# Kernel optimization log

Hardware: AMD Instinct MI355X
Metric: run time of the kernel (lower is better)

## Reference

```python
import jax, jax.numpy as jnp
import numpy as np

B, C, H, W = 2, 512, 64, 64
TC = 256  # transform_channels


def _w(k, o, i):
    return jax.random.normal(k, (o, i), jnp.float32) * (1.0 / np.sqrt(i))


def setup_inputs() -> dict:
    key = jax.random.key(0)
    ks = jax.random.split(key, 8)
    ones = lambda n: jnp.ones((n,), jnp.float32)
    zeros = lambda n: jnp.zeros((n,), jnp.float32)
    return {
        "x": jax.random.normal(ks[0], (B, C, H, W), jnp.float32),
        "q_w1": _w(ks[1], TC, C), "q_g1": ones(TC), "q_b1": zeros(TC),
        "q_w2": _w(ks[2], TC, TC), "q_g2": ones(TC), "q_b2": zeros(TC),
        "k_w1": _w(ks[3], TC, 2 * C), "k_g1": ones(TC), "k_b1": zeros(TC),
        "k_w2": _w(ks[4], TC, TC), "k_g2": ones(TC), "k_b2": zeros(TC),
        "v_w": _w(ks[5], TC, 2 * C), "v_g": ones(TC), "v_b": zeros(TC),
        "o_w": _w(ks[6], C, TC), "o_g": ones(C), "o_b": zeros(C),
    }


def _proj(x, w, g, b):
    """1x1 conv (bias-free) + eval-mode BN (mean=0,var=1 -> per-ch affine) + ReLU.
    x: (B, Cin, N) -> (B, Cout, N)"""
    y = jnp.einsum('oc,bcn->bon', w, x)
    return jax.nn.relu(y * g[None, :, None] + b[None, :, None])


def reference(x, q_w1, q_g1, q_b1, q_w2, q_g2, q_b2,
              k_w1, k_g1, k_b1, k_w2, k_g2, k_b2,
              v_w, v_g, v_b, o_w, o_g, o_b):
    b, c, h, w = x.shape
    n = h * w
    xf = x.reshape(b, c, n)
    # image-level context: spatial softmax * feats, averaged over all positions
    g_vec = jnp.mean(jax.nn.softmax(xf, axis=2) * xf, axis=2)        # (b, c)
    g_map = jnp.broadcast_to(g_vec[:, :, None], (b, c, n))           # 1x1 bilinear upsample == broadcast
    kv_in = jnp.concatenate([g_map, xf], axis=1)                     # (b, 2c, n)

    q = _proj(_proj(xf, q_w1, q_g1, q_b1), q_w2, q_g2, q_b2)         # (b, tc, n)
    k = _proj(_proj(kv_in, k_w1, k_g1, k_b1), k_w2, k_g2, k_b2)      # (b, tc, n)
    v = _proj(kv_in, v_w, v_g, v_b)                                  # (b, tc, n)

    tc = q.shape[1]
    sim = jnp.einsum('bcn,bcm->bnm', q, k) * (tc ** -0.5)            # (b, n, n)
    attn = jax.nn.softmax(sim, axis=-1)
    ctx = jnp.einsum('bnm,bcm->bcn', attn, v)                        # (b, tc, n)
    out = _proj(ctx, o_w, o_g, o_b)                                  # (b, c, n)
    return out.reshape(b, -1, h, w)
```

## Files before the change

### kernel.cpp

```cpp
#include <hip/hip_runtime.h>
#include <stdint.h>

#define DEVINL __device__ __forceinline__

typedef short s16x8 __attribute__((ext_vector_type(8)));
typedef short s16x4 __attribute__((ext_vector_type(4)));
typedef float f32x4 __attribute__((ext_vector_type(4)));
typedef int   i32x4 __attribute__((ext_vector_type(4)));

DEVINL f32x4 MFMA16(s16x8 a, s16x8 b, f32x4 c) {
  return __builtin_amdgcn_mfma_f32_16x16x32_bf16(a, b, c, 0, 0, 0);
}

DEVINL short f2bf(float f) {
  uint32_t u = __float_as_uint(f);
  uint32_t r = (u + 0x7fffu + ((u >> 16) & 1u)) >> 16;
  return (short)r;
}

DEVINL int packbf(float a, float b) {
  return (int)((uint32_t)(uint16_t)f2bf(a) | ((uint32_t)(uint16_t)f2bf(b) << 16));
}

DEVINL void async16(const void* g, void* l) {
  __builtin_amdgcn_global_load_lds(
      (const __attribute__((address_space(1))) void*)g,
      (__attribute__((address_space(3))) void*)l, 16, 0, 0);
}

DEVINL int ab_off(int row, int kg) {
  return ((row * 128 + kg * 16) ^ ((row & 7) << 4)) >> 1;
}
DEVINL int k_off(int key, int dg) {
  return ((key * 512 + dg * 16) ^ ((key & 7) << 4)) >> 1;
}

__global__ __launch_bounds__(256) void prep_kernel(
    const float* __restrict__ x,
    const float* __restrict__ qw1, const float* __restrict__ qw2,
    const float* __restrict__ kw1, const float* __restrict__ kw2,
    const float* __restrict__ vw, const float* __restrict__ ow,
    short* __restrict__ wbuf, short* __restrict__ xt, float* __restrict__ g) {
  __shared__ float t[32][33];
  int gblk = blockIdx.x, tid = threadIdx.x;
  if (gblk < 2560) {
    int idx = gblk * 256 + tid;
    const float* src; int base, stride, coloff, sh, mask;
    if (idx < 131072)      { src = qw1; base = 0;      stride = 512;  coloff = 0;   sh = 9; mask = 511; }
    else if (idx < 196608) { src = qw2; base = 131072; stride = 256;  coloff = 0;   sh = 8; mask = 255; }
    else if (idx < 327680) { src = kw1; base = 196608; stride = 1024; coloff = 512; sh = 9; mask = 511; }
    else if (idx < 393216) { src = kw2; base = 327680; stride = 256;  coloff = 0;   sh = 8; mask = 255; }
    else if (idx < 524288) { src = vw;  base = 393216; stride = 1024; coloff = 512; sh = 9; mask = 511; }
    else                   { src = ow;  base = 524288; stride = 256;  coloff = 0;   sh = 8; mask = 255; }
    int l = idx - base;
    int r = l >> sh, c = l & mask;
    wbuf[idx] = f2bf(src[(size_t)r * stride + coloff + c]);
  } else if (gblk < 6656) {
    int g2 = gblk - 2560;
    int nt = g2 & 127, ct = (g2 >> 7) & 15, b = g2 >> 11;
    int tx = tid & 31, ty = tid >> 5;
    for (int i = 0; i < 4; ++i) {
      int c = ct * 32 + ty + i * 8;
      t[ty + i * 8][tx] = x[((size_t)(b * 512 + c)) * 4096 + nt * 32 + tx];
    }
    __syncthreads();
    for (int i = 0; i < 4; ++i) {
      int n = nt * 32 + ty + i * 8;
      xt[((size_t)(b * 4096 + n)) * 512 + ct * 32 + tx] = f2bf(t[tx][ty + i * 8]);
    }
  } else {
    int g3 = gblk - 6656;
    int c = g3 & 511, b = g3 >> 9;
    const float* row = x + ((size_t)(b * 512 + c)) * 4096;
    int w = tid >> 6, lane = tid & 63;
    float vals[16];
    float vmax = -3e38f;
    for (int i = 0; i < 4; ++i) {
      float4 v = ((const float4*)row)[tid + i * 256];
      vals[i * 4 + 0] = v.x; vals[i * 4 + 1] = v.y;
      vals[i * 4 + 2] = v.z; vals[i * 4 + 3] = v.w;
    }
    for (int i = 0; i < 16; ++i) vmax = fmaxf(vmax, vals[i]);
    for (int off = 1; off < 64; off <<= 1) vmax = fmaxf(vmax, __shfl_xor(vmax, off));
    float* sb = &t[0][0];
    if (lane == 0) sb[w] = vmax;
    __syncthreads();
    vmax = fmaxf(fmaxf(sb[0], sb[1]), fmaxf(sb[2], sb[3]));
    float se = 0.f, sex = 0.f;
    for (int i = 0; i < 16; ++i) {
      float e = __expf(vals[i] - vmax);
      se += e; sex += e * vals[i];
    }
    for (int off = 1; off < 64; off <<= 1) {
      se += __shfl_xor(se, off);
      sex += __shfl_xor(sex, off);
    }
    __syncthreads();
    if (lane == 0) { sb[4 + w] = se; sb[8 + w] = sex; }
    __syncthreads();
    if (tid == 0) {
      float tse = sb[4] + sb[5] + sb[6] + sb[7];
      float tsx = sb[8] + sb[9] + sb[10] + sb[11];
      g[b * 512 + c] = tsx / (tse * 4096.0f);
    }
  }
}

__global__ __launch_bounds__(64) void bias_kernel(const float* __restrict__ kw1,
                                                  const float* __restrict__ vw,
                                                  const float* __restrict__ g,
                                                  float* __restrict__ kbias,
                                                  float* __restrict__ vbias) {
  int o = blockIdx.x, b = blockIdx.y, which = blockIdx.z;
  const float* W = which ? vw : kw1;
  int lane = threadIdx.x;
  float s = 0.f;
  for (int j = 0; j < 8; ++j) {
    int c = lane + j * 64;
    s += W[(size_t)o * 1024 + c] * g[b * 512 + c];
  }
  for (int off = 1; off < 64; off <<= 1) s += __shfl_xor(s, off);
  if (lane == 0) (which ? vbias : kbias)[b * 256 + o] = s;
}

DEVINL void gemm_core(const short* __restrict__ Ap, const short* __restrict__ Bp,
                      int K, short* Alds, short* Blds, int tid,
                      f32x4 (&acc)[4][2]) {
  int lane = tid & 63, w = tid >> 6, lg = lane >> 4, ln = lane & 15;
  int wm = w & 1, wn = w >> 1;
  int nk = K >> 6;
  for (int kt = 0; kt < nk; ++kt) {
    int k0 = kt * 64;
#pragma unroll
    for (int j = 0; j < 4; ++j) {
      int c = tid + j * 256;
      int row = c >> 3, e = c & 7;
      async16(Ap + (size_t)row * K + k0 + ((e ^ (row & 7)) * 8),
              Alds + (size_t)(c & ~63) * 8);
    }
#pragma unroll
    for (int j = 0; j < 2; ++j) {
      int c = tid + j * 256;
      int row = c >> 3, e = c & 7;
      async16(Bp + (size_t)row * K + k0 + ((e ^ (row & 7)) * 8),
              Blds + (size_t)(c & ~63) * 8);
    }
    __syncthreads();
#pragma unroll
    for (int ks = 0; ks < 2; ++ks) {
      s16x8 af[4], bfr[2];
#pragma unroll
      for (int mi = 0; mi < 4; ++mi)
        af[mi] = *(const s16x8*)(Alds + ab_off(wm * 64 + mi * 16 + ln, ks * 4 + lg));
#pragma unroll
      for (int nj = 0; nj < 2; ++nj)
        bfr[nj] = *(const s16x8*)(Blds + ab_off(wn * 32 + nj * 16 + ln, ks * 4 + lg));
#pragma unroll
      for (int mi = 0; mi < 4; ++mi)
#pragma unroll
        for (int nj = 0; nj < 2; ++nj)
          acc[mi][nj] = MFMA16(af[mi], bfr[nj], acc[mi][nj]);
    }
    __syncthreads();
  }
}

__global__ __launch_bounds__(256) void gemm_l1(
    const short* __restrict__ xt,
    const short* __restrict__ WQ1, const short* __restrict__ WK1,
    const short* __restrict__ WV,
    const float* __restrict__ qg1, const float* __restrict__ qb1,
    const float* __restrict__ kg1, const float* __restrict__ kb1,
    const float* __restrict__ vg, const float* __restrict__ vb,
    const float* __restrict__ kbias, const float* __restrict__ vbias,
    short* __restrict__ t1, short* __restrict__ ctxS, short* __restrict__ vbuf) {
  __shared__ alignas(16) short Alds[8192];
  __shared__ alignas(16) short Blds[4096];
  int nt = blockIdx.x, mt = blockIdx.y;
  int gid = blockIdx.z >> 1, b = blockIdx.z & 1;
  const short* A; const float *gm, *bd, *cb; short* out; bool nmode;
  if (gid == 0)      { A = WQ1; gm = qg1; bd = qb1; cb = nullptr; out = t1;   nmode = true; }
  else if (gid == 1) { A = WK1; gm = kg1; bd = kb1; cb = kbias;   out = ctxS; nmode = true; }
  else               { A = WV;  gm = vg;  bd = vb;  cb = vbias;   out = vbuf; nmode = false; }
  int tid = threadIdx.x, lane = tid & 63, w = tid >> 6, lg = lane >> 4, ln = lane & 15;
  int wm = w & 1, wn = w >> 1;
  f32x4 z = {0.f, 0.f, 0.f, 0.f};
  f32x4 acc[4][2];
  for (int mi = 0; mi < 4; ++mi) for (int nj = 0; nj < 2; ++nj) acc[mi][nj] = z;
  gemm_core(A + (size_t)(mt * 128) * 512, xt + ((size_t)b * 4096 + nt * 64) * 512,
            512, Alds, Blds, tid, acc);
  for (int mi = 0; mi < 4; ++mi)
    for (int nj = 0; nj < 2; ++nj) {
      int mbase = mt * 128 + wm * 64 + mi * 16 + lg * 4;
      int n = nt * 64 + wn * 32 + nj * 16 + ln;
      if (nmode) {
        s16x4 pack;
        for (int r = 0; r < 4; ++r) {
          float a = acc[mi][nj][r];
          if (cb) a += cb[b * 256 + mbase + r];
          pack[r] = f2bf(fmaxf(a * gm[mbase + r] + bd[mbase + r], 0.f));
        }
        *(s16x4*)(out + ((size_t)b * 4096 + n) * 256 + mbase) = pack;
      } else {
        for (int r = 0; r < 4; ++r) {
          int m = mbase + r;
          float a = acc[mi][nj][r] + cb[b * 256 + m];
          out[((size_t)(b * 256 + m)) * 4096 + n] = f2bf(fmaxf(a * gm[m] + bd[m], 0.f));
        }
      }
    }
}

__global__ __launch_bounds__(256) void gemm_l2(
    const short* __restrict__ t1, const short* __restrict__ ctxS,
    const short* __restrict__ WQ2, const short* __restrict__ WK2,
    const float* __restrict__ qg2, const float* __restrict__ qb2,
    const float* __restrict__ kg2, const float* __restrict__ kb2,
    short* __restrict__ qbuf, short* __restrict__ kbuf) {
  __shared__ alignas(16) short Alds[8192];
  __shared__ alignas(16) short Blds[4096];
  int nt = blockIdx.x, mt = blockIdx.y;
  int gid = blockIdx.z >> 1, b = blockIdx.z & 1;
  const short* A = gid ? WK2 : WQ2;
  const short* B = gid ? ctxS : t1;
  const float* gm = gid ? kg2 : qg2;
  const float* bd = gid ? kb2 : qb2;
  short* out = gid ? kbuf : qbuf;
  float scale = gid ? 1.0f : 0.0625f;
  int tid = threadIdx.x, lane = tid & 63, w = tid >> 6, lg = lane >> 4, ln = lane & 15;
  int wm = w & 1, wn = w >> 1;
  f32x4 z = {0.f, 0.f, 0.f, 0.f};
  f32x4 acc[4][2];
  for (int mi = 0; mi < 4; ++mi) for (int nj = 0; nj < 2; ++nj) acc[mi][nj] = z;
  gemm_core(A + (size_t)(mt * 128) * 256, B + ((size_t)b * 4096 + nt * 64) * 256,
            256, Alds, Blds, tid, acc);
  for (int mi = 0; mi < 4; ++mi)
    for (int nj = 0; nj < 2; ++nj) {
      int mbase = mt * 128 + wm * 64 + mi * 16 + lg * 4;
      int n = nt * 64 + wn * 32 + nj * 16 + ln;
      s16x4 pack;
      for (int r = 0; r < 4; ++r) {
        float a = acc[mi][nj][r];
        pack[r] = f2bf(fmaxf(a * gm[mbase + r] + bd[mbase + r], 0.f) * scale);
      }
      *(s16x4*)(out + ((size_t)b * 4096 + n) * 256 + mbase) = pack;
    }
}

__global__ __launch_bounds__(256) void gemm_final(
    const short* __restrict__ ctx, const short* __restrict__ WO,
    const float* __restrict__ og, const float* __restrict__ ob,
    float* __restrict__ out) {
  __shared__ alignas(16) short Alds[8192];
  __shared__ alignas(16) short Blds[4096];
  int nt = blockIdx.x, mt = blockIdx.y, b = blockIdx.z;
  int tid = threadIdx.x, lane = tid & 63, w = tid >> 6, lg = lane >> 4, ln = lane & 15;
  int wm = w & 1, wn = w >> 1;
  f32x4 z = {0.f, 0.f, 0.f, 0.f};
  f32x4 acc[4][2];
  for (int mi = 0; mi < 4; ++mi) for (int nj = 0; nj < 2; ++nj) acc[mi][nj] = z;
  gemm_core(WO + (size_t)(mt * 128) * 256, ctx + ((size_t)b * 4096 + nt * 64) * 256,
            256, Alds, Blds, tid, acc);
  for (int mi = 0; mi < 4; ++mi)
    for (int nj = 0; nj < 2; ++nj) {
      int mbase = mt * 128 + wm * 64 + mi * 16 + lg * 4;
      int n = nt * 64 + wn * 32 + nj * 16 + ln;
      for (int r = 0; r < 4; ++r) {
        int m = mbase + r;
        float y = fmaxf(acc[mi][nj][r] * og[m] + ob[m], 0.f);
        out[((size_t)(b * 512 + m)) * 4096 + n] = y;
      }
    }
}

__global__ __launch_bounds__(256, 2) void attn_kernel(
    const short* __restrict__ q, const short* __restrict__ k,
    const short* __restrict__ v, float* __restrict__ accp,
    float* __restrict__ mlp, int nsplit) {
  __shared__ alignas(16) short Klds[8192];
  __shared__ alignas(16) short Vlds[8192];
  __shared__ alignas(16) short Plds[4][512];
  int qt = blockIdx.x, split = blockIdx.y, b = blockIdx.z;
  int tid = threadIdx.x, w = tid >> 6, lane = tid & 63, lg = lane >> 4, ln = lane & 15;

  const short* qrow = q + ((size_t)(b * 4096) + qt * 64 + w * 16 + ln) * 256;
  s16x8 qf[8];
#pragma unroll
  for (int kc = 0; kc < 8; ++kc) qf[kc] = *(const s16x8*)(qrow + kc * 32 + lg * 8);

  f32x4 z = {0.f, 0.f, 0.f, 0.f};
  f32x4 acc[16];
#pragma unroll
  for (int i = 0; i < 16; ++i) acc[i] = z;
  float m_run = -3e38f, l_run = 0.f;

  const size_t kvbase = (size_t)b * 4096 * 256;
  const short* kb_ = k + kvbase;
  const short* vb_ = v + kvbase;
  int kps = 4096 / nsplit;
  int ntiles = kps >> 5;
  int* pw = (int*)&Plds[w][0];

  s16x8 kst[4], vst[4];
  {
    int key0 = split * kps;
#pragma unroll
    for (int j = 0; j < 4; ++j) {
      int c = tid + j * 256;
      kst[j] = *(const s16x8*)(kb_ + (size_t)(key0 + (c >> 5)) * 256 + (c & 31) * 8);
      vst[j] = *(const s16x8*)(vb_ + (size_t)(c >> 2) * 4096 + key0 + (c & 3) * 8);
    }
  }

  for (int tile = 0; tile < ntiles; ++tile) {
#pragma unroll
    for (int j = 0; j < 4; ++j) {
      int c = tid + j * 256;
      *(s16x8*)(Klds + k_off(c >> 5, c & 31)) = kst[j];
      int d = c >> 2, kg = c & 3;
      *(s16x8*)(Vlds + (((kg * 256 + d) ^ ((kg & 1) << 2)) * 8)) = vst[j];
    }
    __syncthreads();
    if (tile + 1 < ntiles) {
      int nk0 = split * kps + (tile + 1) * 32;
#pragma unroll
      for (int j = 0; j < 4; ++j) {
        int c = tid + j * 256;
        kst[j] = *(const s16x8*)(kb_ + (size_t)(nk0 + (c >> 5)) * 256 + (c & 31) * 8);
        vst[j] = *(const s16x8*)(vb_ + (size_t)(c >> 2) * 4096 + nk0 + (c & 3) * 8);
      }
    }
    f32x4 sf0 = z, sf1 = z;
    __builtin_amdgcn_s_setprio(1);
#pragma unroll
    for (int kc = 0; kc < 8; ++kc) {
      s16x8 kb0 = *(const s16x8*)(Klds + k_off(ln, kc * 4 + lg));
      s16x8 kb1 = *(const s16x8*)(Klds + k_off(16 + ln, kc * 4 + lg));
      sf0 = MFMA16(kb0, qf[kc], sf0);
      sf1 = MFMA16(kb1, qf[kc], sf1);
    }
    __builtin_amdgcn_s_setprio(0);
    float mx = fmaxf(fmaxf(fmaxf(sf0[0], sf0[1]), fmaxf(sf0[2], sf0[3])),
                     fmaxf(fmaxf(sf1[0], sf1[1]), fmaxf(sf1[2], sf1[3])));
    mx = fmaxf(mx, __shfl_xor(mx, 16));
    mx = fmaxf(mx, __shfl_xor(mx, 32));
    if (__any(mx > m_run + 8.0f)) {
      float mnew = fmaxf(m_run, mx);
      float alpha = __expf(m_run - mnew);
      m_run = mnew;
      l_run *= alpha;
      float ar0 = __shfl(alpha, lg * 4 + 0);
      float ar1 = __shfl(alpha, lg * 4 + 1);
      float ar2 = __shfl(alpha, lg * 4 + 2);
      float ar3 = __shfl(alpha, lg * 4 + 3);
#pragma unroll
      for (int df = 0; df < 16; ++df) {
        acc[df][0] *= ar0; acc[df][1] *= ar1;
        acc[df][2] *= ar2; acc[df][3] *= ar3;
      }
    }
    float p0[4], p1[4];
    float ps = 0.f;
#pragma unroll
    for (int r = 0; r < 4; ++r) {
      p0[r] = __expf(sf0[r] - m_run);
      p1[r] = __expf(sf1[r] - m_run);
      ps += p0[r] + p1[r];
    }
    ps += __shfl_xor(ps, 16);
    ps += __shfl_xor(ps, 32);
    l_run += ps;
    int u0 = lg ^ (ln & 7);
    int u1 = (4 | lg) ^ (ln & 7);
    *(int2*)(pw + ln * 16 + u0 * 2) = make_int2(packbf(p0[0], p0[1]), packbf(p0[2], p0[3]));
    *(int2*)(pw + ln * 16 + u1 * 2) = make_int2(packbf(p1[0], p1[1]), packbf(p1[2], p1[3]));
    int2 a0 = *(int2*)(pw + ln * 16 + (((2 * lg) ^ (ln & 7)) * 2));
    int2 a1 = *(int2*)(pw + ln * 16 + (((2 * lg + 1) ^ (ln & 7)) * 2));
    i32x4 pt; pt.x = a0.x; pt.y = a0.y; pt.z = a1.x; pt.w = a1.y;
    s16x8 pa = __builtin_bit_cast(s16x8, pt);
    __builtin_amdgcn_s_setprio(1);
#pragma unroll
    for (int df = 0; df < 16; ++df) {
      int unit = (lg * 256 + df * 16 + ln) ^ ((lg & 1) << 2);
      s16x8 vb = *(const s16x8*)(Vlds + unit * 8);
      acc[df] = MFMA16(pa, vb, acc[df]);
    }
    __builtin_amdgcn_s_setprio(0);
    __syncthreads();
  }
  float* accrow = accp + (((size_t)(split * 2 + b) * 4096) + qt * 64 + w * 16) * 256;
#pragma unroll
  for (int df = 0; df < 16; ++df)
#pragma unroll
    for (int r = 0; r < 4; ++r)
      accrow[(size_t)(lg * 4 + r) * 256 + df * 16 + ln] = acc[df][r];
  if (lane < 16) {
    size_t rowi = ((size_t)(split * 2 + b) * 4096) + qt * 64 + w * 16 + ln;
    mlp[rowi * 2] = m_run;
    mlp[rowi * 2 + 1] = l_run;
  }
}

__global__ __launch_bounds__(256) void attn_merge(const float* __restrict__ accp,
                                                  const float* __restrict__ mlp,
                                                  short* __restrict__ ctx, int nsplit) {
  int tid = threadIdx.x;
  int row = blockIdx.x * 4 + (tid >> 6), b = blockIdx.y;
  int lane = tid & 63;
  float M = -3e38f;
  for (int i = 0; i < nsplit; ++i)
    M = fmaxf(M, mlp[((size_t)(i * 2 + b) * 4096 + row) * 2]);
  float denom = 0.f;
  float vx = 0.f, vy = 0.f, vz = 0.f, vw = 0.f;
  for (int i = 0; i < nsplit; ++i) {
    size_t ri = (size_t)(i * 2 + b) * 4096 + row;
    float wgt = __expf(mlp[ri * 2] - M);
    denom += wgt * mlp[ri * 2 + 1];
    float4 a = *(const float4*)(accp + ri * 256 + lane * 4);
    vx += wgt * a.x; vy += wgt * a.y; vz += wgt * a.z; vw += wgt * a.w;
  }
  float inv = 1.0f / denom;
  s16x4 pack;
  pack[0] = f2bf(vx * inv); pack[1] = f2bf(vy * inv);
  pack[2] = f2bf(vz * inv); pack[3] = f2bf(vw * inv);
  *(s16x4*)(ctx + ((size_t)b * 4096 + row) * 256 + lane * 4) = pack;
}

extern "C" void kernel_launch(void* const* d_in, const int* in_sizes, int n_in,
                              void* d_out, int out_size, void* d_ws, size_t ws_size,
                              hipStream_t stream) {
  const float* x    = (const float*)d_in[0];
  const float* qw1  = (const float*)d_in[1];
  const float* qg1  = (const float*)d_in[2];
  const float* qb1  = (const float*)d_in[3];
  const float* qw2  = (const float*)d_in[4];
  const float* qg2  = (const float*)d_in[5];
  const float* qb2  = (const float*)d_in[6];
  const float* kw1  = (const float*)d_in[7];
  const float* kg1  = (const float*)d_in[8];
  const float* kb1f = (const float*)d_in[9];
  const float* kw2  = (const float*)d_in[10];
  const float* kg2  = (const float*)d_in[11];
  const float* kb2f = (const float*)d_in[12];
  const float* vw   = (const float*)d_in[13];
  const float* vg   = (const float*)d_in[14];
  const float* vbf_ = (const float*)d_in[15];
  const float* ow   = (const float*)d_in[16];
  const float* og   = (const float*)d_in[17];
  const float* ob   = (const float*)d_in[18];
  (void)in_sizes; (void)n_in;

  char* ws = (char*)d_ws;
  size_t off = 0;
  short* wbuf = (short*)(ws + off); off += 1310720;
  short* xt   = (short*)(ws + off); off += 8388608;
  float* gvec = (float*)(ws + off); off += 4096;
  float* kbias= (float*)(ws + off); off += 4096;
  float* vbias= (float*)(ws + off); off += 4096;
  short* t1   = (short*)(ws + off); off += 4194304;
  short* qbuf = (short*)(ws + off); off += 4194304;
  short* kbuf = (short*)(ws + off); off += 4194304;
  short* vbuf = (short*)(ws + off); off += 4194304;
  short* ctx  = (short*)(ws + off); off += 4194304;
  float* mlp  = (float*)(ws + off); off += 524288;
  float* accp = (float*)(ws + off);
  size_t basesz = off;
  const size_t per = 8388608ull;
  int nsplit = 1;
  if (ws_size >= basesz + 4 * per) nsplit = 4;
  else if (ws_size >= basesz + 2 * per) nsplit = 2;
  else if (ws_size < basesz + per)
    accp = (float*)d_out;

  prep_kernel<<<7680, 256, 0, stream>>>(x, qw1, qw2, kw1, kw2, vw, ow,
                                        wbuf, xt, gvec);
  bias_kernel<<<dim3(256, 2, 2), 64, 0, stream>>>(kw1, vw, gvec, kbias, vbias);

  short* WQ1 = wbuf + 0;
  short* WQ2 = wbuf + 131072;
  short* WK1 = wbuf + 196608;
  short* WK2 = wbuf + 327680;
  short* WV  = wbuf + 393216;
  short* WO  = wbuf + 524288;

  gemm_l1<<<dim3(64, 2, 6), 256, 0, stream>>>(xt, WQ1, WK1, WV,
                                              qg1, qb1, kg1, kb1f, vg, vbf_,
                                              kbias, vbias, t1, ctx, vbuf);
  gemm_l2<<<dim3(64, 2, 4), 256, 0, stream>>>(t1, ctx, WQ2, WK2,
                                              qg2, qb2, kg2, kb2f, qbuf, kbuf);

  attn_kernel<<<dim3(64, nsplit, 2), 256, 0, stream>>>(qbuf, kbuf, vbuf, accp, mlp, nsplit);
  attn_merge<<<dim3(1024, 2), 256, 0, stream>>>(accp, mlp, ctx, nsplit);

  gemm_final<<<dim3(64, 4, 2), 256, 0, stream>>>(ctx, WO, og, ob, (float*)d_out);
}
```

Baseline: 117.7 us.

## Split PV accumulation by head-dim across waves and double-buffer K/V LDS

After: 120.3 us. 1.02x slower.

```diff
diff --git a/kernel.cpp b/kernel.cpp
--- a/kernel.cpp
+++ b/kernel.cpp
@@ -277,9 +277,11 @@
     const short* __restrict__ q, const short* __restrict__ k,
     const short* __restrict__ v, float* __restrict__ accp,
     float* __restrict__ mlp, int nsplit) {
-  __shared__ alignas(16) short Klds[8192];
-  __shared__ alignas(16) short Vlds[8192];
+  __shared__ alignas(16) short Klds[2][8192];
+  __shared__ alignas(16) short Vlds[2][8192];
   __shared__ alignas(16) short Plds[4][512];
+  __shared__ float alds[4][16];
+  __shared__ int gflag[4];
   int qt = blockIdx.x, split = blockIdx.y, b = blockIdx.z;
   int tid = threadIdx.x, w = tid >> 6, lane = tid & 63, lg = lane >> 4, ln = lane & 15;
 
@@ -289,9 +291,11 @@
   for (int kc = 0; kc < 8; ++kc) qf[kc] = *(const s16x8*)(qrow + kc * 32 + lg * 8);
 
   f32x4 z = {0.f, 0.f, 0.f, 0.f};
-  f32x4 acc[16];
-#pragma unroll
-  for (int i = 0; i < 16; ++i) acc[i] = z;
+  f32x4 acc4[4][4];
+#pragma unroll
+  for (int i = 0; i < 4; ++i)
+#pragma unroll
+    for (int j = 0; j < 4; ++j) acc4[i][j] = z;
   float m_run = -3e38f, l_run = 0.f;
 
   const size_t kvbase = (size_t)b * 4096 * 256;
@@ -312,13 +316,16 @@
     }
   }
 
+  int cur = 0;
   for (int tile = 0; tile < ntiles; ++tile) {
+    short* Kc = &Klds[cur][0];
+    short* Vc = &Vlds[cur][0];
 #pragma unroll
     for (int j = 0; j < 4; ++j) {
       int c = tid + j * 256;
-      *(s16x8*)(Klds + k_off(c >> 5, c & 31)) = kst[j];
+      *(s16x8*)(Kc + k_off(c >> 5, c & 31)) = kst[j];
       int d = c >> 2, kg = c & 3;
-      *(s16x8*)(Vlds + (((kg * 256 + d) ^ ((kg & 1) << 2)) * 8)) = vst[j];
+      *(s16x8*)(Vc + (((kg * 256 + d) ^ ((kg & 1) << 2)) * 8)) = vst[j];
     }
     __syncthreads();
     if (tile + 1 < ntiles) {
@@ -334,8 +341,8 @@
     __builtin_amdgcn_s_setprio(1);
 #pragma unroll
     for (int kc = 0; kc < 8; ++kc) {
-      s16x8 kb0 = *(const s16x8*)(Klds + k_off(ln, kc * 4 + lg));
-      s16x8 kb1 = *(const s16x8*)(Klds + k_off(16 + ln, kc * 4 + lg));
+      s16x8 kb0 = *(const s16x8*)(Kc + k_off(ln, kc * 4 + lg));
+      s16x8 kb1 = *(const s16x8*)(Kc + k_off(16 + ln, kc * 4 + lg));
       sf0 = MFMA16(kb0, qf[kc], sf0);
       sf1 = MFMA16(kb1, qf[kc], sf1);
     }
@@ -344,21 +351,16 @@
                      fmaxf(fmaxf(sf1[0], sf1[1]), fmaxf(sf1[2], sf1[3])));
     mx = fmaxf(mx, __shfl_xor(mx, 16));
     mx = fmaxf(mx, __shfl_xor(mx, 32));
+    float alpha = 1.0f; int grew = 0;
     if (__any(mx > m_run + 8.0f)) {
       float mnew = fmaxf(m_run, mx);
-      float alpha = __expf(m_run - mnew);
+      alpha = __expf(m_run - mnew);
       m_run = mnew;
       l_run *= alpha;
-      float ar0 = __shfl(alpha, lg * 4 + 0);
-      float ar1 = __shfl(alpha, lg * 4 + 1);
-      float ar2 = __shfl(alpha, lg * 4 + 2);
-      float ar3 = __shfl(alpha, lg * 4 + 3);
-#pragma unroll
-      for (int df = 0; df < 16; ++df) {
-        acc[df][0] *= ar0; acc[df][1] *= ar1;
-        acc[df][2] *= ar2; acc[df][3] *= ar3;
-      }
-    }
+      grew = 1;
+    }
+    if (lane < 16) alds[w][ln] = alpha;
+    if (lane == 0) gflag[w] = grew;
     float p0[4], p1[4];
     float ps = 0.f;
 #pragma unroll
@@ -374,26 +376,52 @@
     int u1 = (4 | lg) ^ (ln & 7);
     *(int2*)(pw + ln * 16 + u0 * 2) = make_int2(packbf(p0[0], p0[1]), packbf(p0[2], p0[3]));
     *(int2*)(pw + ln * 16 + u1 * 2) = make_int2(packbf(p1[0], p1[1]), packbf(p1[2], p1[3]));
-    int2 a0 = *(int2*)(pw + ln * 16 + (((2 * lg) ^ (ln & 7)) * 2));
-    int2 a1 = *(int2*)(pw + ln * 16 + (((2 * lg + 1) ^ (ln & 7)) * 2));
-    i32x4 pt; pt.x = a0.x; pt.y = a0.y; pt.z = a1.x; pt.w = a1.y;
-    s16x8 pa = __builtin_bit_cast(s16x8, pt);
+    __syncthreads();
+    if (gflag[0] | gflag[1] | gflag[2] | gflag[3]) {
+#pragma unroll
+      for (int qg = 0; qg < 4; ++qg) {
+        float a0 = alds[qg][lg * 4 + 0];
+        float a1 = alds[qg][lg * 4 + 1];
+        float a2 = alds[qg][lg * 4 + 2];
+        float a3 = alds[qg][lg * 4 + 3];
+#pragma unroll
+        for (int dfl = 0; dfl < 4; ++dfl) {
+          acc4[qg][dfl][0] *= a0; acc4[qg][dfl][1] *= a1;
+          acc4[qg][dfl][2] *= a2; acc4[qg][dfl][3] *= a3;
+        }
+      }
+    }
+    s16x8 paw[4];
+#pragma unroll
+    for (int qg = 0; qg < 4; ++qg) {
+      int* pq = (int*)&Plds[qg][0];
+      int2 a0 = *(int2*)(pq + ln * 16 + (((2 * lg) ^ (ln & 7)) * 2));
+      int2 a1 = *(int2*)(pq + ln * 16 + (((2 * lg + 1) ^ (ln & 7)) * 2));
+      i32x4 pt; pt.x = a0.x; pt.y = a0.y; pt.z = a1.x; pt.w = a1.y;
+      paw[qg] = __builtin_bit_cast(s16x8, pt);
+    }
     __builtin_amdgcn_s_setprio(1);
 #pragma unroll
-    for (int df = 0; df < 16; ++df) {
+    for (int dfl = 0; dfl < 4; ++dfl) {
+      int df = (w << 2) + dfl;
       int unit = (lg * 256 + df * 16 + ln) ^ ((lg & 1) << 2);
-      s16x8 vb = *(const s16x8*)(Vlds + unit * 8);
-      acc[df] = MFMA16(pa, vb, acc[df]);
+      s16x8 vb = *(const s16x8*)(Vc + unit * 8);
+      acc4[0][dfl] = MFMA16(paw[0], vb, acc4[0][dfl]);
+      acc4[1][dfl] = MFMA16(paw[1], vb, acc4[1][dfl]);
+      acc4[2][dfl] = MFMA16(paw[2], vb, acc4[2][dfl]);
+      acc4[3][dfl] = MFMA16(paw[3], vb, acc4[3][dfl]);
     }
     __builtin_amdgcn_s_setprio(0);
-    __syncthreads();
-  }
-  float* accrow = accp + (((size_t)(split * 2 + b) * 4096) + qt * 64 + w * 16) * 256;
-#pragma unroll
-  for (int df = 0; df < 16; ++df)
-#pragma unroll
-    for (int r = 0; r < 4; ++r)
-      accrow[(size_t)(lg * 4 + r) * 256 + df * 16 + ln] = acc[df][r];
+    cur ^= 1;
+  }
+  float* accbase = accp + (((size_t)(split * 2 + b) * 4096) + qt * 64) * 256 + w * 64;
+#pragma unroll
+  for (int qg = 0; qg < 4; ++qg)
+#pragma unroll
+    for (int dfl = 0; dfl < 4; ++dfl)
+#pragma unroll
+      for (int r = 0; r < 4; ++r)
+        accbase[(size_t)(qg * 16 + lg * 4 + r) * 256 + dfl * 16 + ln] = acc4[qg][dfl][r];
   if (lane < 16) {
     size_t rowi = ((size_t)(split * 2 + b) * 4096) + qt * 64 + w * 16 + ln;
     mlp[rowi * 2] = m_run;
```
